# Optimization experiments

Hardware: AMD Instinct MI355X
Metric: run time of the kernel (lower is better)

## Reference

```python
import jax, jax.numpy as jnp
import numpy as np
from jax import lax

K = 3; KK = K * K; S = 1; P = 1; D = 1
BN_EPS = 1e-5


def setup_inputs() -> dict:
    key = jax.random.key(0)
    ks = jax.random.split(key, 4)
    B, C, H, W = 8, 128, 64, 64
    cout = 128
    # xavier-ish scales for conv weights
    def xavier(k, shape):
        fan_in = shape[1] * shape[2] * shape[3]
        fan_out = shape[0] * shape[2] * shape[3]
        limit = np.sqrt(6.0 / (fan_in + fan_out))
        return jax.random.uniform(k, shape, jnp.float32, -limit, limit)
    return {
        "x": jax.random.normal(ks[0], (B, C, H, W), jnp.float32),
        "w_off": xavier(ks[1], (2 * KK, C, K, K)),
        "b_off": jnp.zeros((2 * KK,), jnp.float32),
        "w_mod": xavier(ks[2], (KK, C, K, K)),
        "b_mod": jnp.zeros((KK,), jnp.float32),
        "w_reg": xavier(ks[3], (cout, C, K, K)),
        "b_reg": jnp.zeros((cout,), jnp.float32),
        "gamma": jnp.ones((cout,), jnp.float32),
        "beta": jnp.zeros((cout,), jnp.float32),
    }


def _conv(x, w, b):
    y = lax.conv_general_dilated(x, w, (S, S), [(P, P), (P, P)],
                                 rhs_dilation=(D, D),
                                 dimension_numbers=("NCHW", "OIHW", "NCHW"))
    return y + b[None, :, None, None]


def _deform_conv(x, offset, mask, w_reg, b_reg):
    B, C, H, W = x.shape
    Ho, Wo = offset.shape[2], offset.shape[3]
    # torchvision layout: [B, 2*KK, Ho, Wo], interleaved (dy, dx) per tap
    off = offset.reshape(B, KK, 2, Ho, Wo)
    dy, dx = off[:, :, 0], off[:, :, 1]                      # [B,KK,Ho,Wo]
    ki = jnp.arange(KK) // K
    kj = jnp.arange(KK) % K
    base_y = (jnp.arange(Ho) * S - P)[None, :, None] + (ki * D)[:, None, None]  # [KK,Ho,1]
    base_x = (jnp.arange(Wo) * S - P)[None, None, :] + (kj * D)[:, None, None]  # [KK,1,Wo]
    py = base_y[None].astype(x.dtype) + dy                   # [B,KK,Ho,Wo]
    px = base_x[None].astype(x.dtype) + dx

    y0f = jnp.floor(py); x0f = jnp.floor(px)
    ly = py - y0f; lx = px - x0f
    y0 = y0f.astype(jnp.int32); x0 = x0f.astype(jnp.int32)
    y1 = y0 + 1; x1 = x0 + 1

    def gather(iy, ix):
        valid = ((iy >= 0) & (iy < H) & (ix >= 0) & (ix < W)).astype(x.dtype)
        iyc = jnp.clip(iy, 0, H - 1)
        ixc = jnp.clip(ix, 0, W - 1)
        v = jax.vmap(lambda img, a, b: img[:, a, b])(x, iyc, ixc)  # [B,C,KK,Ho,Wo]
        return v * valid[:, None]

    val = (gather(y0, x0) * ((1 - ly) * (1 - lx))[:, None]
           + gather(y0, x1) * ((1 - ly) * lx)[:, None]
           + gather(y1, x0) * (ly * (1 - lx))[:, None]
           + gather(y1, x1) * (ly * lx)[:, None])               # [B,C,KK,Ho,Wo]

    patches = val * mask[:, None]                               # modulated samples
    wr = w_reg.reshape(w_reg.shape[0], C, KK)
    out = jnp.einsum("ock,bckhw->bohw", wr, patches)
    return out + b_reg[None, :, None, None]


def reference(x, w_off, b_off, w_mod, b_mod, w_reg, b_reg, gamma, beta):
    offset = _conv(x, w_off, b_off)
    modulator = 2.0 * jax.nn.sigmoid(_conv(x, w_mod, b_mod))
    y = _deform_conv(x, offset, modulator, w_reg, b_reg)
    # BatchNorm2d (training-mode batch statistics) + ReLU
    mu = y.mean(axis=(0, 2, 3), keepdims=True)
    var = y.var(axis=(0, 2, 3), keepdims=True)
    y = (y - mu) * lax.rsqrt(var + BN_EPS)
    y = y * gamma[None, :, None, None] + beta[None, :, None, None]
    return jax.nn.relu(y)
```

## Files before the change

### kernel.cpp

```cpp
#include <hip/hip_runtime.h>
#include <math.h>

#define H 64
#define W 64
#define C 128
#define NB 8
#define COUT 128
#define HWi 4096
#define NKC 36
#define PADu 40

typedef __attribute__((ext_vector_type(8))) short short8;
typedef __attribute__((ext_vector_type(8))) unsigned short ushort8;
typedef __attribute__((ext_vector_type(4))) unsigned short ushort4v;
typedef __attribute__((ext_vector_type(4))) float f32x4;

__device__ __forceinline__ unsigned short f2bf(float f){
    unsigned u = __float_as_uint(f);
    unsigned r = (u + 0x7FFFu + ((u >> 16) & 1u)) >> 16;
    return (unsigned short)r;
}
__device__ __forceinline__ float bf2f(unsigned short u){
    return __uint_as_float(((unsigned)u) << 16);
}

__global__ void k_pre(const float* __restrict__ x, unsigned short* __restrict__ xTp,
                      const float* __restrict__ w_reg, const float* __restrict__ w_off,
                      const float* __restrict__ w_mod, const float* __restrict__ b_off,
                      const float* __restrict__ b_mod,
                      unsigned short* __restrict__ wAv, unsigned short* __restrict__ w27A,
                      float* __restrict__ biasom, float* __restrict__ psum){
    int tid = threadIdx.x;
    if (blockIdx.x >= 528){
        int i = (blockIdx.x - 528) * 256 + tid;
        if (i < 147456){
            int kc = i >> 12, rem = i & 4095;
            int q = rem >> 10, r = (rem >> 3) & 127, j = rem & 7;
            int kk = kc * 32 + q * 8 + j, k = kk >> 7, c = kk & 127;
            wAv[i] = f2bf(w_reg[r * 1152 + c * 9 + k]);
        } else if (i < 147456 + 36864){
            int j2 = i - 147456;
            int kc = j2 >> 10, rem = j2 & 1023, m = rem >> 5, kkl = rem & 31;
            int kk = kc * 32 + kkl, k = kk >> 7, c = kk & 127;
            float v = 0.f;
            if (m < 18) v = w_off[m * 1152 + c * 9 + k];
            else if (m < 27) v = w_mod[(m - 18) * 1152 + c * 9 + k];
            w27A[j2] = f2bf(v);
        } else if (i < 147456 + 36864 + 32){
            int m = i - 147456 - 36864;
            biasom[m] = (m < 18) ? b_off[m] : (m < 27 ? b_mod[m - 18] : 0.f);
        } else if (i < 147456 + 36864 + 32 + 256){
            psum[i - 147456 - 36864 - 32] = 0.f;
        }
        return;
    }
    int bidx = blockIdx.x;
    int b = bidx & 7, hp = bidx >> 3;
    unsigned short* row = xTp + (size_t)(b * 66 + hp) * 66 * 128;
    if (hp == 0 || hp == 65){
        ushort8 z = {0,0,0,0,0,0,0,0};
        for (int i = tid; i < 66 * 128 / 8; i += 256) ((ushort8*)row)[i] = z;
        return;
    }
    int h = hp - 1;
    __shared__ unsigned short s[64 * 136];
    int w = tid & 63, c0 = tid >> 6;
    for (int cc = 0; cc < 128; cc += 4){
        int c = cc + c0;
        s[w * 136 + c] = f2bf(x[(size_t)(b * 128 + c) * HWi + h * 64 + w]);
    }
    __syncthreads();
    if (tid < 32){
        ushort8 z = {0,0,0,0,0,0,0,0};
        int wp = (tid < 16) ? 0 : 65;
        int sg = tid & 15;
        *(ushort8*)(row + wp * 128 + sg * 8) = z;
    }
    for (int it = tid; it < 1024; it += 256){
        int w2 = it >> 4, sg = it & 15;
        *(ushort8*)(row + (w2 + 1) * 128 + sg * 8) = *(const ushort8*)(s + w2 * 136 + sg * 8);
    }
}

__global__ __launch_bounds__(256) void k_gemm27(const unsigned short* __restrict__ xTp,
        const unsigned short* __restrict__ w27A, const float* __restrict__ biasom,
        unsigned short* __restrict__ OM){
    __shared__ unsigned short sA[2][32 * PADu];
    __shared__ unsigned short sB[2][64 * PADu];
    int tid = threadIdx.x;
    int lb = (blockIdx.x & 7) * 64 + (blockIdx.x >> 3);
    int n0 = lb * 64;
    int b = n0 >> 12, h = (n0 >> 6) & 63;
    int wv = tid >> 6, lane = tid & 63, quad = lane >> 4, l16 = lane & 15;
    int nl = tid >> 2, sg = tid & 3;
    f32x4 acc0 = {0.f,0.f,0.f,0.f}, acc1 = {0.f,0.f,0.f,0.f};

    ushort8 rA, rB;
    auto loadNext = [&](int kcn){
        int k = kcn >> 2, cb = (kcn & 3) << 5;
        int ki = k / 3, kj = k - ki * 3;
        if (tid < 128) rA = *(const ushort8*)(w27A + kcn * 1024 + tid * 8);
        int rowi = (b * 66 + h + ki) * 66 + (nl + kj);
        rB = *(const ushort8*)(xTp + (size_t)rowi * 128 + cb + sg * 8);
    };
    loadNext(0);
    for (int kc = 0; kc < NKC; kc++){
        int p = kc & 1;
        if (tid < 128) *(ushort8*)(&sA[p][(tid >> 2) * PADu + (tid & 3) * 8]) = rA;
        *(ushort8*)(&sB[p][nl * PADu + sg * 8]) = rB;
        if (kc + 1 < NKC) loadNext(kc + 1);
        __syncthreads();
        short8 bfrag = *(const short8*)(&sB[p][(wv * 16 + l16) * PADu + quad * 8]);
        short8 a0 = *(const short8*)(&sA[p][l16 * PADu + quad * 8]);
        short8 a1 = *(const short8*)(&sA[p][(16 + l16) * PADu + quad * 8]);
        acc0 = __builtin_amdgcn_mfma_f32_16x16x32_bf16(a0, bfrag, acc0, 0, 0, 0);
        acc1 = __builtin_amdgcn_mfma_f32_16x16x32_bf16(a1, bfrag, acc1, 0, 0, 0);
    }
    int n = n0 + wv * 16 + l16;
    #pragma unroll
    for (int t = 0; t < 2; t++){
        f32x4 a = t ? acc1 : acc0;
        ushort4v o;
        #pragma unroll
        for (int r = 0; r < 4; r++){
            int oc = t * 16 + quad * 4 + r;
            float v = a[r] + biasom[oc];
            if (oc >= 18) v = 2.f / (1.f + expf(-v));
            o[r] = f2bf(v);
        }
        *(ushort4v*)(OM + n * 32 + t * 16 + quad * 4) = o;
    }
}

__global__ __launch_bounds__(512, 4) void k_gemm128(const unsigned short* __restrict__ xTp,
        const unsigned short* __restrict__ OM, const unsigned short* __restrict__ wAv,
        const float* __restrict__ b_reg, unsigned short* __restrict__ ybf,
        float* __restrict__ psum){
    __shared__ char smem[49152];
    unsigned short* sA = (unsigned short*)smem;
    unsigned short* sB = (unsigned short*)(smem + 20480);
    int*   s_a0 = (int*)(smem + 30720);
    float* s_w0 = (float*)(smem + 39936);

    int tid = threadIdx.x;
    int lb = (blockIdx.x & 7) * 64 + (blockIdx.x >> 3);
    int n0 = lb * 64;
    int b = n0 >> 12, h = (n0 >> 6) & 63;

    for (int idx = tid; idx < 576; idx += 512){
        int k = idx >> 6, px = idx & 63;
        int n = n0 + px;
        float dy = bf2f(OM[n * 32 + 2 * k]);
        float dx = bf2f(OM[n * 32 + 2 * k + 1]);
        float m  = bf2f(OM[n * 32 + 18 + k]);
        int ki = k / 3, kj = k - ki * 3;
        float py  = (float)(h - 1 + ki) + dy;
        float pxf = (float)(px - 1 + kj) + dx;
        float y0f = floorf(py), x0f = floorf(pxf);
        float ly = py - y0f, lx = pxf - x0f;
        int iy0 = (int)y0f, ix0 = (int)x0f;
        int cy0 = min(max(iy0 + 1, 0), 65), cy1 = min(max(iy0 + 2, 0), 65);
        int cx0 = min(max(ix0 + 1, 0), 65), cx1 = min(max(ix0 + 2, 0), 65);
        int rb = b * 66 * 66;
        s_a0[0 * 576 + idx] = ((rb + cy0 * 66) + cx0) * 128;
        s_a0[1 * 576 + idx] = ((rb + cy0 * 66) + cx1) * 128;
        s_a0[2 * 576 + idx] = ((rb + cy1 * 66) + cx0) * 128;
        s_a0[3 * 576 + idx] = ((rb + cy1 * 66) + cx1) * 128;
        s_w0[0 * 576 + idx] = (1.f - ly) * (1.f - lx) * m;
        s_w0[1 * 576 + idx] = (1.f - ly) * lx * m;
        s_w0[2 * 576 + idx] = ly * (1.f - lx) * m;
        s_w0[3 * 576 + idx] = ly * lx * m;
    }
    __syncthreads();

    int wv = tid >> 6, lane = tid & 63, quad = lane >> 4, l16 = lane & 15;
    int ocq = wv & 3, ng = wv >> 2;
    int rA = tid & 127, qA = tid >> 7;
    int spx = (tid & 255) >> 2, scq = tid & 3;
    bool samp = (tid < 256);

    f32x4 acc00 = {0.f,0.f,0.f,0.f}, acc01 = {0.f,0.f,0.f,0.f};
    f32x4 acc10 = {0.f,0.f,0.f,0.f}, acc11 = {0.f,0.f,0.f,0.f};

    ushort8 rW, rc0, rc1, rc2, rc3;
    float w0 = 0.f, w1 = 0.f, w2 = 0.f, w3 = 0.f;

    auto loadNext = [&](int kcn){
        rW = *(const ushort8*)(wAv + kcn * 4096 + tid * 8);
        if (samp){
            int k = kcn >> 2, cb = (kcn & 3) << 5;
            int idx = k * 64 + spx;
            int co = cb + scq * 8;
            w0 = s_w0[0 * 576 + idx]; w1 = s_w0[1 * 576 + idx];
            w2 = s_w0[2 * 576 + idx]; w3 = s_w0[3 * 576 + idx];
            rc0 = *(const ushort8*)(xTp + s_a0[0 * 576 + idx] + co);
            rc1 = *(const ushort8*)(xTp + s_a0[1 * 576 + idx] + co);
            rc2 = *(const ushort8*)(xTp + s_a0[2 * 576 + idx] + co);
            rc3 = *(const ushort8*)(xTp + s_a0[3 * 576 + idx] + co);
        }
    };
    loadNext(0);
    for (int kc = 0; kc < NKC; kc++){
        int p = kc & 1;
        *(ushort8*)(sA + p * 5120 + rA * PADu + qA * 8) = rW;
        if (samp){
            ushort8 o;
            #pragma unroll
            for (int s = 0; s < 8; s++){
                float v = w0 * bf2f(rc0[s]) + w1 * bf2f(rc1[s])
                        + w2 * bf2f(rc2[s]) + w3 * bf2f(rc3[s]);
                o[s] = f2bf(v);
            }
            *(ushort8*)(sB + p * 2560 + spx * PADu + scq * 8) = o;
        }
        if (kc + 1 < NKC) loadNext(kc + 1);
        __syncthreads();
        const unsigned short* A = sA + p * 5120;
        const unsigned short* Bn = sB + p * 2560;
        short8 a0 = *(const short8*)(A + (ocq * 32 + l16) * PADu + quad * 8);
        short8 a1 = *(const short8*)(A + (ocq * 32 + 16 + l16) * PADu + quad * 8);
        short8 b0 = *(const short8*)(Bn + (ng * 32 + l16) * PADu + quad * 8);
        short8 b1 = *(const short8*)(Bn + (ng * 32 + 16 + l16) * PADu + quad * 8);
        acc00 = __builtin_amdgcn_mfma_f32_16x16x32_bf16(a0, b0, acc00, 0, 0, 0);
        acc01 = __builtin_amdgcn_mfma_f32_16x16x32_bf16(a0, b1, acc01, 0, 0, 0);
        acc10 = __builtin_amdgcn_mfma_f32_16x16x32_bf16(a1, b0, acc10, 0, 0, 0);
        acc11 = __builtin_amdgcn_mfma_f32_16x16x32_bf16(a1, b1, acc11, 0, 0, 0);
    }

    __syncthreads();
    float* ls = (float*)smem;
    int sp0 = h * 64;
    #pragma unroll
    for (int to = 0; to < 2; to++){
        #pragma unroll
        for (int tn = 0; tn < 2; tn++){
            f32x4 a = to ? (tn ? acc11 : acc10) : (tn ? acc01 : acc00);
            int nl = ng * 32 + tn * 16 + l16;
            #pragma unroll
            for (int r = 0; r < 4; r++){
                int oc = ocq * 32 + to * 16 + quad * 4 + r;
                float v = a[r] + b_reg[oc];
                ybf[(size_t)(b * 128 + oc) * HWi + sp0 + nl] = f2bf(v);
                ls[oc * 68 + nl] = v;
            }
        }
    }
    __syncthreads();
    if (tid < 128){
        int oc = tid;
        float s = 0.f, s2 = 0.f;
        #pragma unroll 8
        for (int nl = 0; nl < 64; nl++){
            float v = ls[oc * 68 + nl];
            s += v; s2 = fmaf(v, v, s2);
        }
        atomicAdd(&psum[oc], s);
        atomicAdd(&psum[128 + oc], s2);
    }
}

__global__ void k_apply(const unsigned short* __restrict__ ybf, const float* __restrict__ psum,
                        const float* __restrict__ gamma, const float* __restrict__ beta,
                        float* __restrict__ out){
    int lb = ((int)blockIdx.x & 7) * 256 + ((int)blockIdx.x >> 3);
    int e8 = (lb * 256 + (int)threadIdx.x) * 8;
    int c = (e8 >> 12) & 127;
    ushort8 u = *(const ushort8*)(ybf + e8);
    float s = psum[c], s2 = psum[128 + c];
    float mean = s * (1.f / 32768.f);
    float var  = s2 * (1.f / 32768.f) - mean * mean;
    float rs = rsqrtf(var + 1e-5f);
    float g = gamma[c] * rs;
    float bt = beta[c] - mean * g;
    float4 lo, hi;
    lo.x = fmaxf(fmaf(bf2f(u[0]), g, bt), 0.f);
    lo.y = fmaxf(fmaf(bf2f(u[1]), g, bt), 0.f);
    lo.z = fmaxf(fmaf(bf2f(u[2]), g, bt), 0.f);
    lo.w = fmaxf(fmaf(bf2f(u[3]), g, bt), 0.f);
    hi.x = fmaxf(fmaf(bf2f(u[4]), g, bt), 0.f);
    hi.y = fmaxf(fmaf(bf2f(u[5]), g, bt), 0.f);
    hi.z = fmaxf(fmaf(bf2f(u[6]), g, bt), 0.f);
    hi.w = fmaxf(fmaf(bf2f(u[7]), g, bt), 0.f);
    *(float4*)(out + e8)     = lo;
    *(float4*)(out + e8 + 4) = hi;
}

extern "C" void kernel_launch(void* const* d_in, const int* in_sizes, int n_in,
                              void* d_out, int out_size, void* d_ws, size_t ws_size,
                              hipStream_t stream){
    const float* x     = (const float*)d_in[0];
    const float* w_off = (const float*)d_in[1];
    const float* b_off = (const float*)d_in[2];
    const float* w_mod = (const float*)d_in[3];
    const float* b_mod = (const float*)d_in[4];
    const float* w_reg = (const float*)d_in[5];
    const float* b_reg = (const float*)d_in[6];
    const float* gamma = (const float*)d_in[7];
    const float* beta  = (const float*)d_in[8];

    char* wsb = (char*)d_ws;
    unsigned short* xTp   = (unsigned short*)(wsb);
    unsigned short* OM    = (unsigned short*)(wsb + 8921088);
    unsigned short* ybf   = (unsigned short*)(wsb + 11018240);
    unsigned short* wAv   = (unsigned short*)(wsb + 19406848);
    unsigned short* w27A  = (unsigned short*)(wsb + 19701760);
    float*          biasom= (float*)(wsb + 19775488);
    float*          psum  = (float*)(wsb + 19775616);
    float* out = (float*)d_out;

    hipLaunchKernelGGL(k_pre,    dim3(1250), dim3(256), 0, stream, x, xTp, w_reg, w_off, w_mod, b_off, b_mod, wAv, w27A, biasom, psum);
    hipLaunchKernelGGL(k_gemm27, dim3(512),  dim3(256), 0, stream, xTp, w27A, biasom, OM);
    hipLaunchKernelGGL(k_gemm128,dim3(512),  dim3(512), 0, stream, xTp, OM, wAv, b_reg, ybf, psum);
    hipLaunchKernelGGL(k_apply,  dim3(2048), dim3(256), 0, stream, ybf, psum, gamma, beta, out);
}
```

Baseline: 141.1 us.

## Fuse offset/modulator conv GEMM into deformable GEMM kernel via shared memory

Merges the small offset/mask GEMM kernel into the main deformable-conv GEMM kernel. Its results now pass through shared memory instead of a global OM buffer, which removes one launch and a global round trip. Inside the fused kernel the 512 threads split the 36 K-chunks into two halves of 18, and the partial sums are reduced through shared memory before bias and sigmoid are applied. The cost is that the offset GEMM is now recomputed inside each block of the heavier kernel, which adds barriers and shared-memory reuse that could lengthen each block.

```diff
diff --git a/kernel.cpp b/kernel.cpp
--- a/kernel.cpp
+++ b/kernel.cpp
@@ -82,77 +82,86 @@
     }
 }
 
-__global__ __launch_bounds__(256) void k_gemm27(const unsigned short* __restrict__ xTp,
+__global__ __launch_bounds__(512, 4) void k_fused(const unsigned short* __restrict__ xTp,
         const unsigned short* __restrict__ w27A, const float* __restrict__ biasom,
-        unsigned short* __restrict__ OM){
-    __shared__ unsigned short sA[2][32 * PADu];
-    __shared__ unsigned short sB[2][64 * PADu];
+        const unsigned short* __restrict__ wAv, const float* __restrict__ b_reg,
+        unsigned short* __restrict__ ybf, float* __restrict__ psum){
+    __shared__ char smem[49152];
     int tid = threadIdx.x;
     int lb = (blockIdx.x & 7) * 64 + (blockIdx.x >> 3);
     int n0 = lb * 64;
     int b = n0 >> 12, h = (n0 >> 6) & 63;
-    int wv = tid >> 6, lane = tid & 63, quad = lane >> 4, l16 = lane & 15;
-    int nl = tid >> 2, sg = tid & 3;
-    f32x4 acc0 = {0.f,0.f,0.f,0.f}, acc1 = {0.f,0.f,0.f,0.f};
-
-    ushort8 rA, rB;
-    auto loadNext = [&](int kcn){
-        int k = kcn >> 2, cb = (kcn & 3) << 5;
-        int ki = k / 3, kj = k - ki * 3;
-        if (tid < 128) rA = *(const ushort8*)(w27A + kcn * 1024 + tid * 8);
-        int rowi = (b * 66 + h + ki) * 66 + (nl + kj);
-        rB = *(const ushort8*)(xTp + (size_t)rowi * 128 + cb + sg * 8);
-    };
-    loadNext(0);
-    for (int kc = 0; kc < NKC; kc++){
-        int p = kc & 1;
-        if (tid < 128) *(ushort8*)(&sA[p][(tid >> 2) * PADu + (tid & 3) * 8]) = rA;
-        *(ushort8*)(&sB[p][nl * PADu + sg * 8]) = rB;
-        if (kc + 1 < NKC) loadNext(kc + 1);
+
+    {
+        int grp = tid >> 8, gt = tid & 255;
+        unsigned short* pA = (unsigned short*)(smem + grp * 15360);
+        unsigned short* pB = (unsigned short*)(smem + grp * 15360 + 5120);
+        int wvg = gt >> 6, lane = gt & 63, quad = lane >> 4, l16 = lane & 15;
+        int nl = gt >> 2, sg = gt & 3;
+        f32x4 acc0 = {0.f,0.f,0.f,0.f}, acc1 = {0.f,0.f,0.f,0.f};
+        ushort8 rA, rB;
+        int kc0 = grp * 18;
+        auto p1load = [&](int i){
+            int kc = kc0 + i;
+            int k = kc >> 2, cb = (kc & 3) << 5;
+            int ki = k / 3, kj = k - ki * 3;
+            if (gt < 128) rA = *(const ushort8*)(w27A + kc * 1024 + gt * 8);
+            int rowi = (b * 66 + h + ki) * 66 + (nl + kj);
+            rB = *(const ushort8*)(xTp + (size_t)rowi * 128 + cb + sg * 8);
+        };
+        p1load(0);
+        for (int i = 0; i < 18; i++){
+            int p = i & 1;
+            if (gt < 128) *(ushort8*)(pA + p * 1280 + (gt >> 2) * PADu + (gt & 3) * 8) = rA;
+            *(ushort8*)(pB + p * 2560 + nl * PADu + sg * 8) = rB;
+            if (i + 1 < 18) p1load(i + 1);
+            __syncthreads();
+            short8 bfrag = *(const short8*)(pB + p * 2560 + (wvg * 16 + l16) * PADu + quad * 8);
+            short8 a0 = *(const short8*)(pA + p * 1280 + l16 * PADu + quad * 8);
+            short8 a1 = *(const short8*)(pA + p * 1280 + (16 + l16) * PADu + quad * 8);
+            acc0 = __builtin_amdgcn_mfma_f32_16x16x32_bf16(a0, bfrag, acc0, 0, 0, 0);
+            acc1 = __builtin_amdgcn_mfma_f32_16x16x32_bf16(a1, bfrag, acc1, 0, 0, 0);
+        }
+        float* s_red = (float*)(smem + 30720);
+        int npx = wvg * 16 + l16;
+        if (grp == 1){
+            #pragma unroll
+            for (int t = 0; t < 2; t++){
+                f32x4 a = t ? acc1 : acc0;
+                #pragma unroll
+                for (int r = 0; r < 4; r++)
+                    s_red[npx * 32 + t * 16 + quad * 4 + r] = a[r];
+            }
+        }
         __syncthreads();
-        short8 bfrag = *(const short8*)(&sB[p][(wv * 16 + l16) * PADu + quad * 8]);
-        short8 a0 = *(const short8*)(&sA[p][l16 * PADu + quad * 8]);
-        short8 a1 = *(const short8*)(&sA[p][(16 + l16) * PADu + quad * 8]);
-        acc0 = __builtin_amdgcn_mfma_f32_16x16x32_bf16(a0, bfrag, acc0, 0, 0, 0);
-        acc1 = __builtin_amdgcn_mfma_f32_16x16x32_bf16(a1, bfrag, acc1, 0, 0, 0);
-    }
-    int n = n0 + wv * 16 + l16;
-    #pragma unroll
-    for (int t = 0; t < 2; t++){
-        f32x4 a = t ? acc1 : acc0;
-        ushort4v o;
-        #pragma unroll
-        for (int r = 0; r < 4; r++){
-            int oc = t * 16 + quad * 4 + r;
-            float v = a[r] + biasom[oc];
-            if (oc >= 18) v = 2.f / (1.f + expf(-v));
-            o[r] = f2bf(v);
-        }
-        *(ushort4v*)(OM + n * 32 + t * 16 + quad * 4) = o;
-    }
-}
-
-__global__ __launch_bounds__(512, 4) void k_gemm128(const unsigned short* __restrict__ xTp,
-        const unsigned short* __restrict__ OM, const unsigned short* __restrict__ wAv,
-        const float* __restrict__ b_reg, unsigned short* __restrict__ ybf,
-        float* __restrict__ psum){
-    __shared__ char smem[49152];
+        if (grp == 0){
+            unsigned short* s_OM = (unsigned short*)smem;
+            #pragma unroll
+            for (int t = 0; t < 2; t++){
+                f32x4 a = t ? acc1 : acc0;
+                #pragma unroll
+                for (int r = 0; r < 4; r++){
+                    int oc = t * 16 + quad * 4 + r;
+                    float v = a[r] + s_red[npx * 32 + oc] + biasom[oc];
+                    if (oc >= 18) v = 2.f / (1.f + expf(-v));
+                    s_OM[npx * 32 + oc] = f2bf(v);
+                }
+            }
+        }
+        __syncthreads();
+    }
+
     unsigned short* sA = (unsigned short*)smem;
     unsigned short* sB = (unsigned short*)(smem + 20480);
     int*   s_a0 = (int*)(smem + 30720);
     float* s_w0 = (float*)(smem + 39936);
-
-    int tid = threadIdx.x;
-    int lb = (blockIdx.x & 7) * 64 + (blockIdx.x >> 3);
-    int n0 = lb * 64;
-    int b = n0 >> 12, h = (n0 >> 6) & 63;
+    const unsigned short* s_OM = (const unsigned short*)smem;
 
     for (int idx = tid; idx < 576; idx += 512){
         int k = idx >> 6, px = idx & 63;
-        int n = n0 + px;
-        float dy = bf2f(OM[n * 32 + 2 * k]);
-        float dx = bf2f(OM[n * 32 + 2 * k + 1]);
-        float m  = bf2f(OM[n * 32 + 18 + k]);
+        float dy = bf2f(s_OM[px * 32 + 2 * k]);
+        float dx = bf2f(s_OM[px * 32 + 2 * k + 1]);
+        float m  = bf2f(s_OM[px * 32 + 18 + k]);
         int ki = k / 3, kj = k - ki * 3;
         float py  = (float)(h - 1 + ki) + dy;
         float pxf = (float)(px - 1 + kj) + dx;
@@ -300,7 +309,6 @@
 
     char* wsb = (char*)d_ws;
     unsigned short* xTp   = (unsigned short*)(wsb);
-    unsigned short* OM    = (unsigned short*)(wsb + 8921088);
     unsigned short* ybf   = (unsigned short*)(wsb + 11018240);
     unsigned short* wAv   = (unsigned short*)(wsb + 19406848);
     unsigned short* w27A  = (unsigned short*)(wsb + 19701760);
@@ -308,8 +316,7 @@
     float*          psum  = (float*)(wsb + 19775616);
     float* out = (float*)d_out;
 
-    hipLaunchKernelGGL(k_pre,    dim3(1250), dim3(256), 0, stream, x, xTp, w_reg, w_off, w_mod, b_off, b_mod, wAv, w27A, biasom, psum);
-    hipLaunchKernelGGL(k_gemm27, dim3(512),  dim3(256), 0, stream, xTp, w27A, biasom, OM);
-    hipLaunchKernelGGL(k_gemm128,dim3(512),  dim3(512), 0, stream, xTp, OM, wAv, b_reg, ybf, psum);
-    hipLaunchKernelGGL(k_apply,  dim3(2048), dim3(256), 0, stream, ybf, psum, gamma, beta, out);
-}
+    hipLaunchKernelGGL(k_pre,   dim3(1250), dim3(256), 0, stream, x, xTp, w_reg, w_off, w_mod, b_off, b_mod, wAv, w27A, biasom, psum);
+    hipLaunchKernelGGL(k_fused, dim3(512),  dim3(512), 0, stream, xTp, w27A, biasom, wAv, b_reg, ybf, psum);
+    hipLaunchKernelGGL(k_apply, dim3(2048), dim3(256), 0, stream, ybf, psum, gamma, beta, out);
+}
```

Result: faster. 137.1 us (-2.8%).
